# Kernel tuning notes

Measured on AMD Instinct MI355X. Metric: run time of the kernel, lower is better.

Reference implementation:

```python
import jax, jax.numpy as jnp
import numpy as np

N_NODES = 100000
N_EDGES = 1600000
IN_DIM = 128
HID = 128
OUT = 64


def gcn_conv(x, src, dst, W, b, n_nodes):
    # x: [N, Din] -> [N, Dout]; symmetric-normalized GCN with self-loops (PyG GCNConv defaults)
    h = x @ W  # transform first (as PyG does)
    loop = jnp.arange(n_nodes, dtype=src.dtype)
    s = jnp.concatenate([src, loop])
    d = jnp.concatenate([dst, loop])
    deg = jax.ops.segment_sum(jnp.ones_like(d, dtype=h.dtype), d, num_segments=n_nodes)
    dis = jnp.where(deg > 0, jax.lax.rsqrt(deg), 0.0)
    norm = dis[s] * dis[d]  # [E+N]
    msgs = h[s] * norm[:, None]  # gather-transform
    out = jax.ops.segment_sum(msgs, d, num_segments=n_nodes)  # scatter-add
    return out + b


def setup_inputs() -> dict:
    key = jax.random.key(0)
    ks = jax.random.split(key, 12)
    x = jax.random.normal(ks[0], (N_NODES, IN_DIM), dtype=jnp.float32)
    edge_index = jax.random.randint(ks[1], (2, N_EDGES), 0, N_NODES, dtype=jnp.int32)
    def lin(k, fan_in, fan_out):
        bound = 1.0 / np.sqrt(fan_in)
        kw, kb = jax.random.split(k)
        W = jax.random.uniform(kw, (fan_in, fan_out), minval=-bound, maxval=bound, dtype=jnp.float32)
        b = jax.random.uniform(kb, (fan_out,), minval=-bound, maxval=bound, dtype=jnp.float32)
        return W, b
    W1, b1 = lin(ks[2], IN_DIM, HID)
    W2, b2 = lin(ks[3], HID, HID)
    Wp1, bp1 = lin(ks[4], HID, HID)
    Wp2, bp2 = lin(ks[5], HID, OUT)
    return {"x": x, "edge_index": edge_index,
            "W1": W1, "b1": b1, "W2": W2, "b2": b2,
            "Wp1": Wp1, "bp1": bp1, "Wp2": Wp2, "bp2": bp2}


def reference(x, edge_index, W1, b1, W2, b2, Wp1, bp1, Wp2, bp2):
    n = x.shape[0]
    src, dst = edge_index[0], edge_index[1]
    # layer 1: GCNConv + relu (dropout inactive at eval)
    h = jax.nn.relu(gcn_conv(x, src, dst, W1, b1, n))
    # layer 2
    h = jax.nn.relu(gcn_conv(h, src, dst, W2, b2, n))
    # post MLP head
    h = h @ Wp1 + bp1
    h = h @ Wp2 + bp2
    return jax.nn.log_softmax(h, axis=1)
```

## Files before the change

### kernel.cpp

```cpp
#include <hip/hip_runtime.h>
#include <hip/hip_bf16.h>
#include <cstdint>

typedef __attribute__((ext_vector_type(8))) short short8;
typedef __attribute__((ext_vector_type(16))) float f32x16;
typedef unsigned short us;

#define BIN_SHIFT 9
#define BIN_NODES 512
#define CAPB 12288
#define EPB 4096

__device__ __forceinline__ float bflo(uint32_t u) { return __builtin_bit_cast(float, u << 16); }
__device__ __forceinline__ float bfhi(uint32_t u) { return __builtin_bit_cast(float, u & 0xffff0000u); }

__device__ __forceinline__ us f32_to_bf16_rne(float f) {
  uint32_t u = __builtin_bit_cast(uint32_t, f);
  u += 0x7fffu + ((u >> 16) & 1u);
  return (us)(u >> 16);
}

__device__ __forceinline__ void split2(float f, us& h, us& l) {
  uint32_t u = __builtin_bit_cast(uint32_t, f);
  h = (us)(u >> 16);
  float fh = __builtin_bit_cast(float, u & 0xffff0000u);
  float r = f - fh;
  l = (us)(__builtin_bit_cast(uint32_t, r) >> 16);
}

__global__ __launch_bounds__(256) void k_binA(
    const int* __restrict__ src, const int* __restrict__ dst,
    uint2* __restrict__ binbuf, int* __restrict__ gcur, int E, int nbins) {
  __shared__ uint2 stage[EPB];
  __shared__ int cnt[256], base[256], cur[256], gbase[256];
  int tid = threadIdx.x;
  int e0 = blockIdx.x * EPB;
  int ne = min(EPB, E - e0);
  if (ne <= 0) return;
  cnt[tid] = 0;
  __syncthreads();
  for (int i = tid; i < ne; i += 256) atomicAdd(&cnt[dst[e0 + i] >> BIN_SHIFT], 1);
  __syncthreads();
  if (tid < 64) {
    int carry = 0;
#pragma unroll
    for (int c = 0; c < 4; ++c) {
      int v = cnt[c * 64 + tid];
      int incl = v;
#pragma unroll
      for (int off = 1; off < 64; off <<= 1) {
        int t = __shfl_up(incl, off, 64);
        if (tid >= off) incl += t;
      }
      base[c * 64 + tid] = carry + incl - v;
      carry += __shfl(incl, 63, 64);
    }
  }
  __syncthreads();
  if (tid < nbins && cnt[tid] > 0) gbase[tid] = atomicAdd(&gcur[tid], cnt[tid]);
  cur[tid] = base[tid];
  __syncthreads();
  for (int i = tid; i < ne; i += 256) {
    int d = dst[e0 + i], s = src[e0 + i];
    int p = atomicAdd(&cur[d >> BIN_SHIFT], 1);
    stage[p] = make_uint2((unsigned)d, (unsigned)s);
  }
  __syncthreads();
  for (int i = tid; i < ne; i += 256) {
    uint2 en = stage[i];
    int b = en.x >> BIN_SHIFT;
    int gi = gbase[b] + (i - base[b]);
    if (gi < CAPB) binbuf[(size_t)b * CAPB + gi] = en;
  }
}

__global__ __launch_bounds__(256) void k_passB(
    const uint2* __restrict__ binbuf, const int* __restrict__ gcur,
    int* __restrict__ deg, float* __restrict__ dis, int* __restrict__ start,
    int* __restrict__ col, int N, int nbins) {
  __shared__ int hist[512], lstart[512], cur[512];
  __shared__ int colstage[CAPB];
  __shared__ int binbase_s;
  int b = blockIdx.x, tid = threadIdx.x;
  int node0 = b << BIN_SHIFT;
  int cnt = min(gcur[b], CAPB);
  hist[tid] = 0; hist[tid + 256] = 0;
  __syncthreads();
  const uint2* bp = binbuf + (size_t)b * CAPB;
  for (int i = tid; i < cnt; i += 256) atomicAdd(&hist[bp[i].x & (BIN_NODES - 1)], 1);
  __syncthreads();
  if (tid < 64) {
    int s = 0;
    for (int i = tid; i < b; i += 64) s += min(gcur[i], CAPB);
#pragma unroll
    for (int off = 32; off; off >>= 1) s += __shfl_xor(s, off, 64);
    if (tid == 0) binbase_s = s;
    int carry = 0;
#pragma unroll
    for (int c = 0; c < 8; ++c) {
      int v = hist[c * 64 + tid];
      int incl = v;
#pragma unroll
      for (int off = 1; off < 64; off <<= 1) {
        int t = __shfl_up(incl, off, 64);
        if (tid >= off) incl += t;
      }
      lstart[c * 64 + tid] = carry + incl - v;
      carry += __shfl(incl, 63, 64);
    }
  }
  __syncthreads();
  int binbase = binbase_s;
  for (int i = tid; i < 512; i += 256) {
    int node = node0 + i;
    if (node < N) {
      int dg = hist[i];
      deg[node] = dg;
      dis[node] = rsqrtf((float)(dg + 1));
      start[node] = binbase + lstart[i];
    }
  }
  cur[tid] = lstart[tid]; cur[tid + 256] = lstart[tid + 256];
  __syncthreads();
  for (int i = tid; i < cnt; i += 256) {
    uint2 en = bp[i];
    int p = atomicAdd(&cur[en.x & (BIN_NODES - 1)], 1);
    colstage[p] = (int)en.y;
  }
  __syncthreads();
  for (int i = tid; i < cnt; i += 256) col[binbase + i] = colstage[i];
}

__global__ void k_prep(const float* __restrict__ W1, const float* __restrict__ W2,
                       const float* __restrict__ Wp1, const float* __restrict__ Wp2,
                       const float* __restrict__ bp1, const float* __restrict__ bp2,
                       us* __restrict__ Wt1h, us* __restrict__ Wt1l,
                       us* __restrict__ Wt2h, us* __restrict__ Wt2l,
                       us* __restrict__ Wch, us* __restrict__ Wcl, float* __restrict__ bc) {
  int blk = blockIdx.x, tid = threadIdx.x;
  if (blk < 128) {
    const float* W = (blk < 64) ? W1 : W2;
    us* Wh = (blk < 64) ? Wt1h : Wt2h;
    us* Wl = (blk < 64) ? Wt1l : Wt2l;
    int idx = (blk & 63) * 256 + tid;
    int k = idx >> 7, n = idx & 127;
    us h, l;
    split2(W[idx], h, l);
    Wh[n * 128 + k] = h;
    Wl[n * 128 + k] = l;
  } else if (blk < 160) {
    int idx = (blk - 128) * 256 + tid;
    int k = idx >> 6, j = idx & 63;
    float acc = 0.f;
    for (int t = 0; t < 128; ++t) acc += Wp1[k * 128 + t] * Wp2[t * 64 + j];
    us h, l;
    split2(acc, h, l);
    Wch[j * 128 + k] = h;
    Wcl[j * 128 + k] = l;
  } else {
    int j = tid;
    if (j < 64) {
      float acc = bp2[j];
      for (int t = 0; t < 128; ++t) acc += bp1[t] * Wp2[t * 64 + j];
      bc[j] = acc;
    }
  }
}

template <bool AF32>
__global__ __launch_bounds__(256) void k_gemm_mfma(
    const void* __restrict__ Av, const us* __restrict__ Wh,
    const us* __restrict__ Wl, const float* __restrict__ dis,
    us* __restrict__ out_bf16, int N, int ntiles) {
  __shared__ us As_hi[32 * 136];
  __shared__ us As_lo[32 * 136];
  int tid = threadIdx.x;
  int wave = tid >> 6, lane = tid & 63;
  int n0 = wave * 32;
  int nn = n0 + (lane & 31);
  int khalf = (lane >> 5) * 8;
  int m = lane & 31;

  short8 bh[8], bl[8];
#pragma unroll
  for (int c = 0; c < 8; ++c) {
    bh[c] = *(const short8*)&Wh[nn * 128 + c * 16 + khalf];
    bl[c] = *(const short8*)&Wl[nn * 128 + c * 16 + khalf];
  }

  for (int t = blockIdx.x; t < ntiles; t += gridDim.x) {
    int row0 = t * 32;
    __syncthreads();
    if (AF32) {
      const float* A = (const float*)Av;
      for (int j = tid; j < 1024; j += 256) {
        int r = j >> 5, c = j & 31;
        int row = row0 + r;
        float4 v = make_float4(0.f, 0.f, 0.f, 0.f);
        if (row < N) v = *(const float4*)&A[(size_t)row * 128 + c * 4];
        us h0, h1, h2, h3, l0, l1, l2, l3;
        split2(v.x, h0, l0); split2(v.y, h1, l1);
        split2(v.z, h2, l2); split2(v.w, h3, l3);
        *(ushort4*)&As_hi[r * 136 + c * 4] = make_ushort4(h0, h1, h2, h3);
        *(ushort4*)&As_lo[r * 136 + c * 4] = make_ushort4(l0, l1, l2, l3);
      }
    } else {
      const us* A = (const us*)Av;
      for (int j = tid; j < 512; j += 256) {
        int r = j >> 4, c = j & 15;
        int row = row0 + r;
        uint4 v = make_uint4(0u, 0u, 0u, 0u);
        if (row < N) v = *(const uint4*)&A[(size_t)row * 128 + c * 8];
        *(uint4*)&As_hi[r * 136 + c * 8] = v;
      }
    }
    __syncthreads();

    f32x16 acc = {};
#pragma unroll
    for (int c = 0; c < 8; ++c) {
      short8 ah = *(const short8*)&As_hi[m * 136 + c * 16 + khalf];
      acc = __builtin_amdgcn_mfma_f32_32x32x16_bf16(ah, bh[c], acc, 0, 0, 0);
      acc = __builtin_amdgcn_mfma_f32_32x32x16_bf16(ah, bl[c], acc, 0, 0, 0);
      if (AF32) {
        short8 al = *(const short8*)&As_lo[m * 136 + c * 16 + khalf];
        acc = __builtin_amdgcn_mfma_f32_32x32x16_bf16(al, bh[c], acc, 0, 0, 0);
      }
    }

    int col = n0 + (lane & 31);
    int rbase = row0 + 4 * (lane >> 5);
#pragma unroll
    for (int reg = 0; reg < 16; ++reg) {
      int row = rbase + (reg & 3) + 8 * (reg >> 2);
      if (row < N) {
        float v = acc[reg] * dis[row];
        out_bf16[(size_t)row * 128 + col] = f32_to_bf16_rne(v);
      }
    }
  }
}

__global__ __launch_bounds__(256) void k_gather(
    const us* __restrict__ h, us* __restrict__ o,
    const int* __restrict__ start, const int* __restrict__ deg,
    const int* __restrict__ col, const float* __restrict__ dis,
    const float* __restrict__ bias, int N) {
  int tid = threadIdx.x;
  int node = blockIdx.x * 8 + (tid >> 5);
  int lane = tid & 31;
  if (node >= N) return;
  const uint2* h2 = (const uint2*)h;
  uint2 u = h2[(size_t)node * 32 + lane];
  float ax = bflo(u.x), ay = bfhi(u.x), az = bflo(u.y), aw = bfhi(u.y);
  int e = start[node];
  int e_end = e + deg[node];
  for (; e + 1 < e_end; e += 2) {
    uint2 u1 = h2[(size_t)col[e] * 32 + lane];
    uint2 u2 = h2[(size_t)col[e + 1] * 32 + lane];
    ax += bflo(u1.x) + bflo(u2.x); ay += bfhi(u1.x) + bfhi(u2.x);
    az += bflo(u1.y) + bflo(u2.y); aw += bfhi(u1.y) + bfhi(u2.y);
  }
  if (e < e_end) {
    uint2 u1 = h2[(size_t)col[e] * 32 + lane];
    ax += bflo(u1.x); ay += bfhi(u1.x); az += bflo(u1.y); aw += bfhi(u1.y);
  }
  float sc = dis[node];
  float4 b = ((const float4*)bias)[lane];
  float rx = fmaxf(ax * sc + b.x, 0.f);
  float ry = fmaxf(ay * sc + b.y, 0.f);
  float rz = fmaxf(az * sc + b.z, 0.f);
  float rw = fmaxf(aw * sc + b.w, 0.f);
  uint2 po;
  po.x = ((uint32_t)f32_to_bf16_rne(ry) << 16) | f32_to_bf16_rne(rx);
  po.y = ((uint32_t)f32_to_bf16_rne(rw) << 16) | f32_to_bf16_rne(rz);
  ((uint2*)o)[(size_t)node * 32 + lane] = po;
}

__global__ __launch_bounds__(256) void k_head_mfma(
    const us* __restrict__ act, const us* __restrict__ Wch,
    const us* __restrict__ Wcl, const float* __restrict__ bc,
    float* __restrict__ out, int N) {
  __shared__ us As[64 * 136];
  __shared__ float red[2][2][64];
  int tid = threadIdx.x;
  int wave = tid >> 6, lane = tid & 63;
  int rt = wave >> 1, ct = wave & 1;
  int colj = ct * 32 + (lane & 31);
  int khalf = (lane >> 5) * 8;
  int m = lane & 31;

  short8 bh[8], bl[8];
#pragma unroll
  for (int c = 0; c < 8; ++c) {
    bh[c] = *(const short8*)&Wch[colj * 128 + c * 16 + khalf];
    bl[c] = *(const short8*)&Wcl[colj * 128 + c * 16 + khalf];
  }

  int row0 = blockIdx.x * 64;
  for (int j = tid; j < 1024; j += 256) {
    int r = j >> 4, c = j & 15;
    int row = row0 + r;
    uint4 v = make_uint4(0u, 0u, 0u, 0u);
    if (row < N) v = *(const uint4*)&act[(size_t)row * 128 + c * 8];
    *(uint4*)&As[r * 136 + c * 8] = v;
  }
  __syncthreads();

  f32x16 acc = {};
  int mrow = rt * 32 + m;
#pragma unroll
  for (int c = 0; c < 8; ++c) {
    short8 ah = *(const short8*)&As[mrow * 136 + c * 16 + khalf];
    acc = __builtin_amdgcn_mfma_f32_32x32x16_bf16(ah, bh[c], acc, 0, 0, 0);
    acc = __builtin_amdgcn_mfma_f32_32x32x16_bf16(ah, bl[c], acc, 0, 0, 0);
  }

  float bcv = bc[colj];
  float lg[16], mx[16];
#pragma unroll
  for (int reg = 0; reg < 16; ++reg) {
    lg[reg] = acc[reg] + bcv;
    float v = lg[reg];
#pragma unroll
    for (int off = 16; off > 0; off >>= 1) v = fmaxf(v, __shfl_xor(v, off, 32));
    mx[reg] = v;
  }
  if ((lane & 31) == 0) {
#pragma unroll
    for (int reg = 0; reg < 16; ++reg) {
      int rl = rt * 32 + (reg & 3) + 8 * (reg >> 2) + 4 * (lane >> 5);
      red[0][ct][rl] = mx[reg];
    }
  }
  __syncthreads();

  float ex[16], sm[16];
#pragma unroll
  for (int reg = 0; reg < 16; ++reg) {
    int rl = rt * 32 + (reg & 3) + 8 * (reg >> 2) + 4 * (lane >> 5);
    float rmax = fmaxf(red[0][0][rl], red[0][1][rl]);
    ex[reg] = lg[reg] - rmax;
    float v = expf(ex[reg]);
#pragma unroll
    for (int off = 16; off > 0; off >>= 1) v += __shfl_xor(v, off, 32);
    sm[reg] = v;
  }
  if ((lane & 31) == 0) {
#pragma unroll
    for (int reg = 0; reg < 16; ++reg) {
      int rl = rt * 32 + (reg & 3) + 8 * (reg >> 2) + 4 * (lane >> 5);
      red[1][ct][rl] = sm[reg];
    }
  }
  __syncthreads();

#pragma unroll
  for (int reg = 0; reg < 16; ++reg) {
    int rl = rt * 32 + (reg & 3) + 8 * (reg >> 2) + 4 * (lane >> 5);
    int row = row0 + rl;
    if (row < N) {
      float total = red[1][0][rl] + red[1][1][rl];
      out[(size_t)row * 64 + colj] = ex[reg] - logf(total);
    }
  }
}

extern "C" void kernel_launch(void* const* d_in, const int* in_sizes, int n_in,
                              void* d_out, int out_size, void* d_ws, size_t ws_size,
                              hipStream_t stream) {
  const float* x   = (const float*)d_in[0];
  const int*   ei  = (const int*)d_in[1];
  const float* W1  = (const float*)d_in[2];
  const float* b1  = (const float*)d_in[3];
  const float* W2  = (const float*)d_in[4];
  const float* b2  = (const float*)d_in[5];
  const float* Wp1 = (const float*)d_in[6];
  const float* bp1 = (const float*)d_in[7];
  const float* Wp2 = (const float*)d_in[8];
  const float* bp2 = (const float*)d_in[9];
  float* out = (float*)d_out;

  int N = in_sizes[0] / 128;
  int E = in_sizes[1] / 2;
  const int* src = ei;
  const int* dst = ei + E;
  int nbins = (N + BIN_NODES - 1) >> BIN_SHIFT;

  float* dis   = (float*)d_ws;
  int*   deg   = (int*)(dis + N);
  int*   start = deg + N;
  int*   col   = start + N;
  int*   gcur  = col + ((E + 3) & ~3);
  us* Wt1h = (us*)(gcur + 256);
  us* Wt1l = Wt1h + 16384;
  us* Wt2h = Wt1l + 16384;
  us* Wt2l = Wt2h + 16384;
  us* Wch  = Wt2l + 16384;
  us* Wcl  = Wch + 8192;
  float* bc = (float*)(Wcl + 8192);
  uint2* binbuf = (uint2*)(bc + 80);
  us* hbuf = (us*)(binbuf + (size_t)nbins * CAPB);
  us* act  = hbuf + (size_t)N * 128;

  hipMemsetAsync(gcur, 0, 256 * sizeof(int), stream);

  int ablocks = (E + EPB - 1) / EPB;
  k_binA<<<ablocks, 256, 0, stream>>>(src, dst, binbuf, gcur, E, nbins);
  k_passB<<<nbins, 256, 0, stream>>>(binbuf, gcur, deg, dis, start, col, N, nbins);
  k_prep<<<161, 256, 0, stream>>>(W1, W2, Wp1, Wp2, bp1, bp2,
                                  Wt1h, Wt1l, Wt2h, Wt2l, Wch, Wcl, bc);

  int ntiles = (N + 31) / 32;
  int gemm_grid = ntiles < 1024 ? ntiles : 1024;
  int agblocks = (N + 7) / 8;
  int hblocks = (N + 63) / 64;

  k_gemm_mfma<true><<<gemm_grid, 256, 0, stream>>>(x, Wt1h, Wt1l, dis, hbuf, N, ntiles);
  k_gather<<<agblocks, 256, 0, stream>>>(hbuf, act, start, deg, col, dis, b1, N);
  k_gemm_mfma<false><<<gemm_grid, 256, 0, stream>>>(act, Wt2h, Wt2l, dis, hbuf, N, ntiles);
  k_gather<<<agblocks, 256, 0, stream>>>(hbuf, act, start, deg, col, dis, b2, N);
  k_head_mfma<<<hblocks, 256, 0, stream>>>(act, Wch, Wcl, bc, out, N);
}
```

Before: 409.4 us.

## Gather with one wave per node, loading neighbor indices once and broadcasting via readlane

The aggregation kernel now assigns a full 64-lane wave to each node, with each lane holding two bf16 features. It loads up to 64 neighbor indices with a single coalesced load and broadcasts them with readlane, unrolled four-wide with independent accumulators. Out-of-range slots point to an extra zeroed padding row of h, so the loop needs no per-edge bounds checks. This removes the repeated scalar col loads and raises memory-level parallelism, at the cost of more wasted lanes on low-degree nodes and extra padding rows read when the degree is not a multiple of four.

```diff
diff --git a/kernel.cpp b/kernel.cpp
--- a/kernel.cpp
+++ b/kernel.cpp
@@ -246,35 +246,41 @@
     const int* __restrict__ start, const int* __restrict__ deg,
     const int* __restrict__ col, const float* __restrict__ dis,
     const float* __restrict__ bias, int N) {
-  int tid = threadIdx.x;
-  int node = blockIdx.x * 8 + (tid >> 5);
-  int lane = tid & 31;
+  int wave = threadIdx.x >> 6, lane = threadIdx.x & 63;
+  int node = blockIdx.x * 4 + wave;
   if (node >= N) return;
-  const uint2* h2 = (const uint2*)h;
-  uint2 u = h2[(size_t)node * 32 + lane];
-  float ax = bflo(u.x), ay = bfhi(u.x), az = bflo(u.y), aw = bfhi(u.y);
-  int e = start[node];
-  int e_end = e + deg[node];
-  for (; e + 1 < e_end; e += 2) {
-    uint2 u1 = h2[(size_t)col[e] * 32 + lane];
-    uint2 u2 = h2[(size_t)col[e + 1] * 32 + lane];
-    ax += bflo(u1.x) + bflo(u2.x); ay += bfhi(u1.x) + bfhi(u2.x);
-    az += bflo(u1.y) + bflo(u2.y); aw += bfhi(u1.y) + bfhi(u2.y);
-  }
-  if (e < e_end) {
-    uint2 u1 = h2[(size_t)col[e] * 32 + lane];
-    ax += bflo(u1.x); ay += bfhi(u1.x); az += bflo(u1.y); aw += bfhi(u1.y);
+  const uint32_t* h1 = (const uint32_t*)h;
+  uint32_t u = h1[(size_t)node * 64 + lane];
+  float a0 = bflo(u), b0 = bfhi(u);
+  float a1 = 0.f, b1 = 0.f, a2 = 0.f, b2 = 0.f, a3 = 0.f, b3 = 0.f;
+  int e0 = start[node];
+  int dg = deg[node];
+  int myc = (lane < dg) ? col[e0 + lane] : N;
+  int dgm = min(dg, 64);
+  for (int k = 0; k < dgm; k += 4) {
+    int c0 = __builtin_amdgcn_readlane(myc, k);
+    int c1 = __builtin_amdgcn_readlane(myc, k + 1);
+    int c2 = __builtin_amdgcn_readlane(myc, k + 2);
+    int c3 = __builtin_amdgcn_readlane(myc, k + 3);
+    uint32_t u0 = h1[(size_t)c0 * 64 + lane];
+    uint32_t u1 = h1[(size_t)c1 * 64 + lane];
+    uint32_t u2 = h1[(size_t)c2 * 64 + lane];
+    uint32_t u3 = h1[(size_t)c3 * 64 + lane];
+    a0 += bflo(u0); b0 += bfhi(u0);
+    a1 += bflo(u1); b1 += bfhi(u1);
+    a2 += bflo(u2); b2 += bfhi(u2);
+    a3 += bflo(u3); b3 += bfhi(u3);
+  }
+  for (int e = e0 + 64; e < e0 + dg; ++e) {
+    uint32_t u0 = h1[(size_t)col[e] * 64 + lane];
+    a0 += bflo(u0); b0 += bfhi(u0);
   }
   float sc = dis[node];
-  float4 b = ((const float4*)bias)[lane];
-  float rx = fmaxf(ax * sc + b.x, 0.f);
-  float ry = fmaxf(ay * sc + b.y, 0.f);
-  float rz = fmaxf(az * sc + b.z, 0.f);
-  float rw = fmaxf(aw * sc + b.w, 0.f);
-  uint2 po;
-  po.x = ((uint32_t)f32_to_bf16_rne(ry) << 16) | f32_to_bf16_rne(rx);
-  po.y = ((uint32_t)f32_to_bf16_rne(rw) << 16) | f32_to_bf16_rne(rz);
-  ((uint2*)o)[(size_t)node * 32 + lane] = po;
+  float2 bb = ((const float2*)bias)[lane];
+  float rx = fmaxf((a0 + a1 + a2 + a3) * sc + bb.x, 0.f);
+  float ry = fmaxf((b0 + b1 + b2 + b3) * sc + bb.y, 0.f);
+  ((uint32_t*)o)[(size_t)node * 64 + lane] =
+      ((uint32_t)f32_to_bf16_rne(ry) << 16) | f32_to_bf16_rne(rx);
 }
 
 __global__ __launch_bounds__(256) void k_head_mfma(
@@ -401,9 +407,10 @@
   float* bc = (float*)(Wcl + 8192);
   uint2* binbuf = (uint2*)(bc + 80);
   us* hbuf = (us*)(binbuf + (size_t)nbins * CAPB);
-  us* act  = hbuf + (size_t)N * 128;
+  us* act  = hbuf + (size_t)(N + 1) * 128;
 
   hipMemsetAsync(gcur, 0, 256 * sizeof(int), stream);
+  hipMemsetAsync(hbuf + (size_t)N * 128, 0, 128 * sizeof(us), stream);
 
   int ablocks = (E + EPB - 1) / EPB;
   k_binA<<<ablocks, 256, 0, stream>>>(src, dst, binbuf, gcur, E, nbins);
@@ -413,7 +420,7 @@
 
   int ntiles = (N + 31) / 32;
   int gemm_grid = ntiles < 1024 ? ntiles : 1024;
-  int agblocks = (N + 7) / 8;
+  int agblocks = (N + 3) / 4;
   int hblocks = (N + 63) / 64;
 
   k_gemm_mfma<true><<<gemm_grid, 256, 0, stream>>>(x, Wt1h, Wt1l, dis, hbuf, N, ntiles);
```

Result: no change. 402.5 us (-1.7%).
